# Kernel optimization log

Measured on AMD Instinct MI355X. Metric: run time of the kernel, lower is better.

Reference implementation:

```python
import jax, jax.numpy as jnp
import numpy as np

B, N, C, H = 4, 2048, 1024, 16
D = C // H  # head_dim


def setup_inputs() -> dict:
    key = jax.random.key(0)
    ks = jax.random.split(key, 9)
    s = 1.0 / np.sqrt(C)
    return {
        "x": jax.random.normal(ks[0], (B, N, C), dtype=jnp.float32),
        "Wq": jax.random.uniform(ks[1], (C, C), jnp.float32, -s, s),
        "bq": jax.random.uniform(ks[2], (C,), jnp.float32, -s, s),
        "Wk": jax.random.uniform(ks[3], (C, C), jnp.float32, -s, s),
        "bk": jax.random.uniform(ks[4], (C,), jnp.float32, -s, s),
        "Wv": jax.random.uniform(ks[5], (C, C), jnp.float32, -s, s),
        "bv": jax.random.uniform(ks[6], (C,), jnp.float32, -s, s),
        "Wo": jax.random.uniform(ks[7], (C, C), jnp.float32, -s, s),
        "bo": jax.random.uniform(ks[8], (C,), jnp.float32, -s, s),
    }


def reference(x, Wq, bq, Wk, bk, Wv, bv, Wo, bo):
    # QKV projections -> [B, H, N, D]
    def proj(W, b):
        y = jnp.einsum('bnc,cd->bnd', x, W) + b
        return y.reshape(B, N, H, D).transpose(0, 2, 1, 3)

    q = proj(Wq, bq)
    k = proj(Wk, bk)
    v = proj(Wv, bv)

    scale = 1.0 / np.sqrt(D).astype(np.float32)
    scores = jnp.einsum('bhnd,bhmd->bhnm', q, k) * scale  # [B,H,N,N]
    probs = jax.nn.softmax(scores, axis=-1)
    out = jnp.einsum('bhnm,bhmd->bhnd', probs, v)  # [B,H,N,D]
    out = out.transpose(0, 2, 1, 3).reshape(B, N, C)
    return jnp.einsum('bnc,cd->bnd', out, Wo) + bo
```

## Files before the change

### kernel.cpp

```cpp
#include <hip/hip_runtime.h>
#include <hip/hip_bf16.h>
#include <stdint.h>


#define DEV __device__ __forceinline__

typedef unsigned short u16;
typedef __attribute__((ext_vector_type(8))) _Float16 f16x8;
typedef __attribute__((ext_vector_type(4))) float f32x4;

static constexpr int NB = 4, NN = 2048, NC = 1024, NH = 16, ND = 64;

DEV u16 f2h(float f) {
    _Float16 h = (_Float16)f;
    return __builtin_bit_cast(u16, h);
}

#define GLD16(gp, lp)                                                         \
    __builtin_amdgcn_global_load_lds(                                         \
        (__attribute__((address_space(1))) void*)(gp),                        \
        (__attribute__((address_space(3))) void*)(lp), 16, 0, 0)

DEV f32x4 mfma16(f16x8 a, f16x8 b, f32x4 c) {
    return __builtin_amdgcn_mfma_f32_16x16x32_f16(a, b, c, 0, 0, 0);
}

__global__ void cast_fuse(const float* __restrict__ x,
                          const float* __restrict__ Wq, const float* __restrict__ Wk,
                          const float* __restrict__ Wv, const float* __restrict__ Wo,
                          u16* __restrict__ xb, u16* __restrict__ Wt4) {
    __shared__ float lds[64 * 68];
    int bid = blockIdx.x, tid = threadIdx.x;
    if (bid < 4096) {
        size_t base = (size_t)bid * 2048 + (size_t)tid * 8;
        float4 v0 = *(const float4*)(x + base);
        float4 v1 = *(const float4*)(x + base + 4);
        union { u16 u[8]; uint4 v; } p;
        p.u[0] = f2h(v0.x); p.u[1] = f2h(v0.y); p.u[2] = f2h(v0.z); p.u[3] = f2h(v0.w);
        p.u[4] = f2h(v1.x); p.u[5] = f2h(v1.y); p.u[6] = f2h(v1.z); p.u[7] = f2h(v1.w);
        *(uint4*)(xb + base) = p.v;
        return;
    }
    bid -= 4096;
    int wsel = bid >> 8, t = bid & 255;
    int k0 = (t >> 4) * 64, n0 = (t & 15) * 64;
    const float* W = wsel == 0 ? Wq : wsel == 1 ? Wk : wsel == 2 ? Wv : Wo;
    u16* Wt = Wt4 + (size_t)wsel * 1048576;
#pragma unroll
    for (int i = 0; i < 4; i++) {
        int slot = tid * 4 + i * 1024;
        int rr = slot >> 6, cc = slot & 63;
        float4 v = *(const float4*)(W + (size_t)(k0 + rr) * 1024 + n0 + cc);
        *(float4*)(&lds[rr * 68 + cc]) = v;
    }
    __syncthreads();
    int n = tid >> 2, kc = (tid & 3) * 16;
    union { u16 u[16]; uint4 v[2]; } p;
#pragma unroll
    for (int j = 0; j < 16; j++) p.u[j] = f2h(lds[(kc + j) * 68 + n]);
    u16* dst = Wt + (size_t)(n0 + n) * 1024 + k0 + kc;
    *(uint4*)(dst) = p.v[0];
    *(uint4*)(dst + 8) = p.v[1];
}

DEV void gemm_core(const u16* __restrict__ A, const u16* __restrict__ Wt,
                   int m0, int n0, f32x4 (&acc)[4][4]) {
    __shared__ u16 Alds[128 * 32];
    __shared__ u16 Blds[128 * 32];
    const int tid = threadIdx.x, lane = tid & 63;
    const int w = tid >> 6, g = lane >> 4, r16 = lane & 15;
    const int wm = (w >> 1) * 64, wn = (w & 1) * 64;
#pragma unroll
    for (int i = 0; i < 4; i++)
#pragma unroll
        for (int j = 0; j < 4; j++) acc[i][j] = f32x4{0.f, 0.f, 0.f, 0.f};

    for (int kt = 0; kt < 32; ++kt) {
        int k0 = kt * 32;
#pragma unroll
        for (int i = 0; i < 2; i++) {
            int slot = i * 4096 + tid * 16;
            int rr = slot >> 6, cc = slot & 63;
            GLD16((const char*)A + (size_t)(m0 + rr) * 2048 + k0 * 2 + cc,
                  (char*)Alds + slot);
            GLD16((const char*)Wt + (size_t)(n0 + rr) * 2048 + k0 * 2 + cc,
                  (char*)Blds + slot);
        }
        __syncthreads();
        f16x8 af[4], bf[4];
#pragma unroll
        for (int i = 0; i < 4; i++) {
            af[i] = *(const f16x8*)((const char*)Alds + (wm + i * 16 + r16) * 64 + g * 16);
            bf[i] = *(const f16x8*)((const char*)Blds + (wn + i * 16 + r16) * 64 + g * 16);
        }
#pragma unroll
        for (int i = 0; i < 4; i++)
#pragma unroll
            for (int j = 0; j < 4; j++) acc[i][j] = mfma16(af[i], bf[j], acc[i][j]);
        __syncthreads();
    }
}

__global__ __launch_bounds__(256, 2) void gemm_qkv(
    const u16* __restrict__ xb, const u16* __restrict__ Wt4,
    const float* __restrict__ bq, const float* __restrict__ bk,
    const float* __restrict__ bv,
    u16* __restrict__ Qo, u16* __restrict__ Ko, u16* __restrict__ Vo) {
    int m0 = blockIdx.x * 128, n0 = blockIdx.y * 128, z = blockIdx.z;
    const u16* Wt = Wt4 + (size_t)z * 1048576;
    const float* bias = z == 0 ? bq : z == 1 ? bk : bv;
    u16* Out = z == 0 ? Qo : z == 1 ? Ko : Vo;
    f32x4 acc[4][4];
    gemm_core(xb, Wt, m0, n0, acc);
    const int lane = threadIdx.x & 63, w = threadIdx.x >> 6;
    const int g = lane >> 4, r16 = lane & 15;
    const int wm = (w >> 1) * 64, wn = (w & 1) * 64;
#pragma unroll
    for (int j = 0; j < 4; j++) {
        int c = n0 + wn + j * 16 + r16;
        float bb = bias[c];
        int h = c >> 6, d = c & 63;
#pragma unroll
        for (int i = 0; i < 4; i++) {
#pragma unroll
            for (int rr = 0; rr < 4; rr++) {
                int m = m0 + wm + i * 16 + g * 4 + rr;
                int b = m >> 11, n = m & 2047;
                Out[(((size_t)(b * 16 + h)) * 2048 + n) * 64 + d] = f2h(acc[i][j][rr] + bb);
            }
        }
    }
}

__global__ __launch_bounds__(256, 2) void gemm_out(
    const u16* __restrict__ AO, const u16* __restrict__ Wt,
    const float* __restrict__ bo, float* __restrict__ Out) {
    int m0 = blockIdx.x * 128, n0 = blockIdx.y * 128;
    f32x4 acc[4][4];
    gemm_core(AO, Wt, m0, n0, acc);
    const int lane = threadIdx.x & 63, w = threadIdx.x >> 6;
    const int g = lane >> 4, r16 = lane & 15;
    const int wm = (w >> 1) * 64, wn = (w & 1) * 64;
#pragma unroll
    for (int j = 0; j < 4; j++) {
        int c = n0 + wn + j * 16 + r16;
        float bb = bo[c];
#pragma unroll
        for (int i = 0; i < 4; i++) {
#pragma unroll
            for (int rr = 0; rr < 4; rr++) {
                int m = m0 + wm + i * 16 + g * 4 + rr;
                Out[(size_t)m * 1024 + c] = acc[i][j][rr] + bb;
            }
        }
    }
}

__global__ void transpose_v(const u16* __restrict__ V, u16* __restrict__ VT) {
    __shared__ u16 lds[64 * 66];
    int bh = blockIdx.x >> 5, n0 = (blockIdx.x & 31) * 64;
    const u16* Vb = V + (size_t)bh * 2048 * 64;
    u16* VTb = VT + (size_t)bh * 64 * 2048;
    int tid = threadIdx.x;
#pragma unroll
    for (int i = 0; i < 8; i++) {
        int p = tid + i * 256;
        int rr = p >> 5, c2 = (p & 31) * 2;
        unsigned int val = *(const unsigned int*)(Vb + (size_t)(n0 + rr) * 64 + c2);
        *(unsigned int*)(&lds[rr * 66 + c2]) = val;
    }
    __syncthreads();
#pragma unroll
    for (int i = 0; i < 2; i++) {
        int s = tid * 8 + i * 2048;
        int d = s >> 6, ns = s & 63;
        union { u16 u[8]; uint4 v; } p;
#pragma unroll
        for (int j = 0; j < 8; j++) p.u[j] = lds[(ns + j) * 66 + d];
        *(uint4*)(VTb + (size_t)d * 2048 + n0 + ns) = p.v;
    }
}

__global__ __launch_bounds__(256, 2) void attn_k(
    const u16* __restrict__ Q, const u16* __restrict__ K,
    const u16* __restrict__ VT, u16* __restrict__ AO) {
    __shared__ char Klds[8192];
    __shared__ char Vlds[8192];
    __shared__ char Plds[4][4096];
    const int bh = blockIdx.x, q0 = blockIdx.y * 128;
    const int tid = threadIdx.x, lane = tid & 63, w = tid >> 6;
    const int g = lane >> 4, r16 = lane & 15;
    const char* Qb = (const char*)(Q + (size_t)bh * 2048 * 64);
    const char* Kb = (const char*)(K + (size_t)bh * 2048 * 64);
    const char* VTb = (const char*)(VT + (size_t)bh * 64 * 2048);

    f16x8 qf[2][2];
#pragma unroll
    for (int qg = 0; qg < 2; qg++)
#pragma unroll
        for (int ks = 0; ks < 2; ks++)
            qf[qg][ks] = *(const f16x8*)(Qb + (size_t)(q0 + w * 32 + qg * 16 + r16) * 128 +
                                         ks * 64 + g * 16);
    f32x4 oacc[2][4];
#pragma unroll
    for (int qg = 0; qg < 2; qg++)
#pragma unroll
        for (int dg = 0; dg < 4; dg++) oacc[qg][dg] = f32x4{0.f, 0.f, 0.f, 0.f};
    float mrun[2] = {-1e30f, -1e30f}, lrun[2] = {0.f, 0.f};

    for (int t = 0; t < 32; ++t) {
#pragma unroll
        for (int i = 0; i < 2; i++) {
            int slot = i * 4096 + tid * 16;
            int rr = slot >> 7, cc = slot & 127;
            int sw = cc ^ ((rr & 7) << 4);
            GLD16(Kb + (size_t)(t * 64 + rr) * 128 + sw, Klds + slot);
            GLD16(VTb + (size_t)rr * 4096 + t * 128 + sw, Vlds + slot);
        }
        __syncthreads();

        f32x4 sacc[4][2];
#pragma unroll
        for (int kg = 0; kg < 4; kg++)
#pragma unroll
            for (int qg = 0; qg < 2; qg++) sacc[kg][qg] = f32x4{0.f, 0.f, 0.f, 0.f};
#pragma unroll
        for (int kg = 0; kg < 4; kg++) {
#pragma unroll
            for (int ks = 0; ks < 2; ks++) {
                int row = kg * 16 + r16;
                f16x8 kf = *(const f16x8*)(Klds + row * 128 +
                                           ((ks * 64 + g * 16) ^ ((row & 7) << 4)));
#pragma unroll
                for (int qg = 0; qg < 2; qg++)
                    sacc[kg][qg] = mfma16(kf, qf[qg][ks], sacc[kg][qg]);
            }
        }

#pragma unroll
        for (int qg = 0; qg < 2; qg++) {
            float pm = -1e30f;
#pragma unroll
            for (int kg = 0; kg < 4; kg++)
#pragma unroll
                for (int rr = 0; rr < 4; rr++) pm = fmaxf(pm, sacc[kg][qg][rr]);
            pm = fmaxf(pm, __shfl_xor(pm, 16));
            pm = fmaxf(pm, __shfl_xor(pm, 32));
            pm *= 0.125f;
            float mn = fmaxf(mrun[qg], pm);
            float fsc = exp2f((mrun[qg] - mn) * 1.44269504f);
            mrun[qg] = mn;
            float nm = -mn * 1.44269504f;
            float rs = 0.f;
#pragma unroll
            for (int kg = 0; kg < 4; kg++) {
                union { u16 u[4]; uint2 v; } pk;
#pragma unroll
                for (int rr = 0; rr < 4; rr++) {
                    float p = exp2f(fmaf(sacc[kg][qg][rr], 0.18033688f, nm));
                    rs += p;
                    pk.u[rr] = f2h(p);
                }
                int byte = (qg * 16 + r16) * 128 + ((kg * 32 + g * 8) ^ ((r16 & 7) << 4));
                *(uint2*)(&Plds[w][byte]) = pk.v;
            }
            rs += __shfl_xor(rs, 16);
            rs += __shfl_xor(rs, 32);
            lrun[qg] = lrun[qg] * fsc + rs;
            float fr[4];
#pragma unroll
            for (int rr = 0; rr < 4; rr++) fr[rr] = __shfl(fsc, g * 4 + rr);
#pragma unroll
            for (int dg = 0; dg < 4; dg++)
#pragma unroll
                for (int rr = 0; rr < 4; rr++) oacc[qg][dg][rr] *= fr[rr];
        }

#pragma unroll
        for (int ks = 0; ks < 2; ks++) {
            f16x8 pf[2], vf[4];
#pragma unroll
            for (int qg = 0; qg < 2; qg++) {
                int row = qg * 16 + r16;
                pf[qg] = *(const f16x8*)(Plds[w] + row * 128 +
                                         ((ks * 64 + g * 16) ^ ((r16 & 7) << 4)));
            }
#pragma unroll
            for (int dg = 0; dg < 4; dg++) {
                int row = dg * 16 + r16;
                vf[dg] = *(const f16x8*)(Vlds + row * 128 +
                                         ((ks * 64 + g * 16) ^ ((r16 & 7) << 4)));
            }
#pragma unroll
            for (int qg = 0; qg < 2; qg++)
#pragma unroll
                for (int dg = 0; dg < 4; dg++)
                    oacc[qg][dg] = mfma16(pf[qg], vf[dg], oacc[qg][dg]);
        }
        __syncthreads();
    }

    const int b = bh >> 4, h = bh & 15;
#pragma unroll
    for (int qg = 0; qg < 2; qg++) {
        float linv = 1.0f / lrun[qg];
        float lr[4];
#pragma unroll
        for (int rr = 0; rr < 4; rr++) lr[rr] = __shfl(linv, g * 4 + rr);
#pragma unroll
        for (int dg = 0; dg < 4; dg++) {
            int d = dg * 16 + r16;
#pragma unroll
            for (int rr = 0; rr < 4; rr++) {
                int nrow = q0 + w * 32 + qg * 16 + g * 4 + rr;
                AO[((size_t)(b * 2048 + nrow)) * 1024 + h * 64 + d] =
                    f2h(oacc[qg][dg][rr] * lr[rr]);
            }
        }
    }
}

extern "C" void kernel_launch(void* const* d_in, const int* in_sizes, int n_in,
                              void* d_out, int out_size, void* d_ws, size_t ws_size,
                              hipStream_t stream) {
    const float* x = (const float*)d_in[0];
    const float* Wq = (const float*)d_in[1];
    const float* bq = (const float*)d_in[2];
    const float* Wk = (const float*)d_in[3];
    const float* bk = (const float*)d_in[4];
    const float* Wv = (const float*)d_in[5];
    const float* bv = (const float*)d_in[6];
    const float* Wo = (const float*)d_in[7];
    const float* bo = (const float*)d_in[8];

    char* ws = (char*)d_ws;
    u16* xb  = (u16*)(ws);
    u16* Wt  = (u16*)(ws + (16ull << 20));
    u16* Qb  = (u16*)(ws + (24ull << 20));
    u16* Kb  = (u16*)(ws + (40ull << 20));
    u16* Vb  = (u16*)(ws + (56ull << 20));
    u16* VTb = (u16*)(ws + (72ull << 20));
    u16* AO  = (u16*)(ws + (88ull << 20));

    cast_fuse<<<dim3(5120), dim3(256), 0, stream>>>(x, Wq, Wk, Wv, Wo, xb, Wt);
    gemm_qkv<<<dim3(64, 8, 3), dim3(256), 0, stream>>>(xb, Wt, bq, bk, bv, Qb, Kb, Vb);
    transpose_v<<<dim3(2048), dim3(256), 0, stream>>>(Vb, VTb);
    attn_k<<<dim3(64, 16), dim3(256), 0, stream>>>(Qb, Kb, VTb, AO);
    gemm_out<<<dim3(64, 8), dim3(256), 0, stream>>>(AO, Wt + 3ull * 1048576, bo,
                                                    (float*)d_out);
}
```

Baseline: 345.1 us.

## Double-buffer GEMM and attention tiles, widen KV tile, lazy softmax rescale

Both the projection GEMM core and the attention kernel now stage the next tile into a second LDS buffer while computing on the current one, so there is only one barrier per iteration. The attention kernel processes 128 keys per step and raises wave priority around the MFMA sections. It rescales the running max and output only when some row's max grows by more than a threshold. The 1/sqrt(D) scale is folded into the Q projection epilogue. The cost is more LDS per block (about 80 KB for attention), which may limit occupancy, and extra register pressure from the larger score tile.

```diff
diff --git a/kernel.cpp b/kernel.cpp
--- a/kernel.cpp
+++ b/kernel.cpp
@@ -8,8 +8,6 @@
 typedef unsigned short u16;
 typedef __attribute__((ext_vector_type(8))) _Float16 f16x8;
 typedef __attribute__((ext_vector_type(4))) float f32x4;
-
-static constexpr int NB = 4, NN = 2048, NC = 1024, NH = 16, ND = 64;
 
 DEV u16 f2h(float f) {
     _Float16 h = (_Float16)f;
@@ -65,8 +63,8 @@
 
 DEV void gemm_core(const u16* __restrict__ A, const u16* __restrict__ Wt,
                    int m0, int n0, f32x4 (&acc)[4][4]) {
-    __shared__ u16 Alds[128 * 32];
-    __shared__ u16 Blds[128 * 32];
+    __shared__ u16 Alds[2][128 * 32];
+    __shared__ u16 Blds[2][128 * 32];
     const int tid = threadIdx.x, lane = tid & 63;
     const int w = tid >> 6, g = lane >> 4, r16 = lane & 15;
     const int wm = (w >> 1) * 64, wn = (w & 1) * 64;
@@ -75,23 +73,29 @@
 #pragma unroll
         for (int j = 0; j < 4; j++) acc[i][j] = f32x4{0.f, 0.f, 0.f, 0.f};
 
-    for (int kt = 0; kt < 32; ++kt) {
-        int k0 = kt * 32;
+    auto stage = [&](int buf, int kt) {
+        int k0 = kt * 64;
 #pragma unroll
         for (int i = 0; i < 2; i++) {
             int slot = i * 4096 + tid * 16;
             int rr = slot >> 6, cc = slot & 63;
-            GLD16((const char*)A + (size_t)(m0 + rr) * 2048 + k0 * 2 + cc,
-                  (char*)Alds + slot);
-            GLD16((const char*)Wt + (size_t)(n0 + rr) * 2048 + k0 * 2 + cc,
-                  (char*)Blds + slot);
-        }
-        __syncthreads();
+            GLD16((const char*)A + (size_t)(m0 + rr) * 2048 + k0 + cc,
+                  (char*)Alds[buf] + slot);
+            GLD16((const char*)Wt + (size_t)(n0 + rr) * 2048 + k0 + cc,
+                  (char*)Blds[buf] + slot);
+        }
+    };
+    stage(0, 0);
+    __syncthreads();
+
+    for (int kt = 0; kt < 32; ++kt) {
+        int cur = kt & 1;
+        if (kt < 31) stage(cur ^ 1, kt + 1);
         f16x8 af[4], bf[4];
 #pragma unroll
         for (int i = 0; i < 4; i++) {
-            af[i] = *(const f16x8*)((const char*)Alds + (wm + i * 16 + r16) * 64 + g * 16);
-            bf[i] = *(const f16x8*)((const char*)Blds + (wn + i * 16 + r16) * 64 + g * 16);
+            af[i] = *(const f16x8*)((const char*)Alds[cur] + (wm + i * 16 + r16) * 64 + g * 16);
+            bf[i] = *(const f16x8*)((const char*)Blds[cur] + (wn + i * 16 + r16) * 64 + g * 16);
         }
 #pragma unroll
         for (int i = 0; i < 4; i++)
@@ -110,6 +114,7 @@
     const u16* Wt = Wt4 + (size_t)z * 1048576;
     const float* bias = z == 0 ? bq : z == 1 ? bk : bv;
     u16* Out = z == 0 ? Qo : z == 1 ? Ko : Vo;
+    const float sc = (z == 0) ? 0.125f : 1.0f;
     f32x4 acc[4][4];
     gemm_core(xb, Wt, m0, n0, acc);
     const int lane = threadIdx.x & 63, w = threadIdx.x >> 6;
@@ -126,7 +131,8 @@
             for (int rr = 0; rr < 4; rr++) {
                 int m = m0 + wm + i * 16 + g * 4 + rr;
                 int b = m >> 11, n = m & 2047;
-                Out[(((size_t)(b * 16 + h)) * 2048 + n) * 64 + d] = f2h(acc[i][j][rr] + bb);
+                Out[(((size_t)(b * 16 + h)) * 2048 + n) * 64 + d] =
+                    f2h((acc[i][j][rr] + bb) * sc);
             }
         }
     }
@@ -184,8 +190,8 @@
 __global__ __launch_bounds__(256, 2) void attn_k(
     const u16* __restrict__ Q, const u16* __restrict__ K,
     const u16* __restrict__ VT, u16* __restrict__ AO) {
-    __shared__ char Klds[8192];
-    __shared__ char Vlds[8192];
+    __shared__ char Klds[2][16384];
+    __shared__ char Vlds[2][16384];
     __shared__ char Plds[4][4096];
     const int bh = blockIdx.x, q0 = blockIdx.y * 128;
     const int tid = threadIdx.x, lane = tid & 63, w = tid >> 6;
@@ -193,6 +199,8 @@
     const char* Qb = (const char*)(Q + (size_t)bh * 2048 * 64);
     const char* Kb = (const char*)(K + (size_t)bh * 2048 * 64);
     const char* VTb = (const char*)(VT + (size_t)bh * 64 * 2048);
+    char* Pw = Plds[w];
+    const f32x4 ZZ = {0.f, 0.f, 0.f, 0.f};
 
     f16x8 qf[2][2];
 #pragma unroll
@@ -205,98 +213,128 @@
 #pragma unroll
     for (int qg = 0; qg < 2; qg++)
 #pragma unroll
-        for (int dg = 0; dg < 4; dg++) oacc[qg][dg] = f32x4{0.f, 0.f, 0.f, 0.f};
+        for (int dg = 0; dg < 4; dg++) oacc[qg][dg] = ZZ;
     float mrun[2] = {-1e30f, -1e30f}, lrun[2] = {0.f, 0.f};
 
-    for (int t = 0; t < 32; ++t) {
-#pragma unroll
-        for (int i = 0; i < 2; i++) {
+    auto stage = [&](int buf, int t) {
+#pragma unroll
+        for (int i = 0; i < 4; i++) {
             int slot = i * 4096 + tid * 16;
-            int rr = slot >> 7, cc = slot & 127;
-            int sw = cc ^ ((rr & 7) << 4);
-            GLD16(Kb + (size_t)(t * 64 + rr) * 128 + sw, Klds + slot);
-            GLD16(VTb + (size_t)rr * 4096 + t * 128 + sw, Vlds + slot);
-        }
-        __syncthreads();
-
-        f32x4 sacc[4][2];
-#pragma unroll
-        for (int kg = 0; kg < 4; kg++)
-#pragma unroll
-            for (int qg = 0; qg < 2; qg++) sacc[kg][qg] = f32x4{0.f, 0.f, 0.f, 0.f};
-#pragma unroll
-        for (int kg = 0; kg < 4; kg++) {
-#pragma unroll
-            for (int ks = 0; ks < 2; ks++) {
-                int row = kg * 16 + r16;
-                f16x8 kf = *(const f16x8*)(Klds + row * 128 +
-                                           ((ks * 64 + g * 16) ^ ((row & 7) << 4)));
-#pragma unroll
-                for (int qg = 0; qg < 2; qg++)
-                    sacc[kg][qg] = mfma16(kf, qf[qg][ks], sacc[kg][qg]);
-            }
-        }
-
+            {
+                int rr = slot >> 7, cc = slot & 127;
+                GLD16(Kb + (size_t)(t * 128 + rr) * 128 + (cc ^ ((rr & 7) << 4)),
+                      Klds[buf] + slot);
+            }
+            {
+                int rr = slot >> 8, cc = slot & 255;
+                GLD16(VTb + (size_t)rr * 4096 + t * 256 + (cc ^ ((rr & 7) << 4)),
+                      Vlds[buf] + slot);
+            }
+        }
+    };
+    stage(0, 0);
+    __syncthreads();
+
+    for (int t = 0; t < 16; ++t) {
+        const int cur = t & 1;
+        if (t < 15) stage(cur ^ 1, t + 1);
+        const char* Kl = Klds[cur];
+        const char* Vl = Vlds[cur];
+
+        f32x4 sacc[8][2];
+        __builtin_amdgcn_s_setprio(1);
+#pragma unroll
+        for (int kg = 0; kg < 8; kg++) {
+            int row = kg * 16 + r16, sw = (row & 7) << 4;
+            f16x8 kf0 = *(const f16x8*)(Kl + row * 128 + ((g * 16) ^ sw));
+            f16x8 kf1 = *(const f16x8*)(Kl + row * 128 + ((64 + g * 16) ^ sw));
+#pragma unroll
+            for (int qg = 0; qg < 2; qg++) {
+                sacc[kg][qg] = mfma16(kf0, qf[qg][0], ZZ);
+                sacc[kg][qg] = mfma16(kf1, qf[qg][1], sacc[kg][qg]);
+            }
+        }
+        __builtin_amdgcn_s_setprio(0);
+
+        float pmv[2];
 #pragma unroll
         for (int qg = 0; qg < 2; qg++) {
             float pm = -1e30f;
 #pragma unroll
-            for (int kg = 0; kg < 4; kg++)
+            for (int kg = 0; kg < 8; kg++)
 #pragma unroll
                 for (int rr = 0; rr < 4; rr++) pm = fmaxf(pm, sacc[kg][qg][rr]);
             pm = fmaxf(pm, __shfl_xor(pm, 16));
             pm = fmaxf(pm, __shfl_xor(pm, 32));
-            pm *= 0.125f;
-            float mn = fmaxf(mrun[qg], pm);
-            float fsc = exp2f((mrun[qg] - mn) * 1.44269504f);
-            mrun[qg] = mn;
-            float nm = -mn * 1.44269504f;
-            float rs = 0.f;
-#pragma unroll
-            for (int kg = 0; kg < 4; kg++) {
-                union { u16 u[4]; uint2 v; } pk;
-#pragma unroll
-                for (int rr = 0; rr < 4; rr++) {
-                    float p = exp2f(fmaf(sacc[kg][qg][rr], 0.18033688f, nm));
-                    rs += p;
-                    pk.u[rr] = f2h(p);
+            pmv[qg] = pm;
+        }
+        if (__any(fmaxf(pmv[0] - mrun[0], pmv[1] - mrun[1]) > 8.0f)) {
+#pragma unroll
+            for (int qg = 0; qg < 2; qg++) {
+                float mn = fmaxf(mrun[qg], pmv[qg]);
+                float fsc = exp2f((mrun[qg] - mn) * 1.44269504f);
+                mrun[qg] = mn;
+                lrun[qg] *= fsc;
+                float fr[4];
+#pragma unroll
+                for (int rr = 0; rr < 4; rr++) fr[rr] = __shfl(fsc, g * 4 + rr);
+#pragma unroll
+                for (int dg = 0; dg < 4; dg++)
+#pragma unroll
+                    for (int rr = 0; rr < 4; rr++) oacc[qg][dg][rr] *= fr[rr];
+            }
+        }
+
+        float rs[2] = {0.f, 0.f};
+#pragma unroll
+        for (int h = 0; h < 2; h++) {
+#pragma unroll
+            for (int qg = 0; qg < 2; qg++) {
+                float nm = -mrun[qg] * 1.44269504f;
+#pragma unroll
+                for (int kg2 = 0; kg2 < 4; kg2++) {
+                    int kg = h * 4 + kg2;
+                    union { u16 u[4]; uint2 v; } pk;
+#pragma unroll
+                    for (int rr = 0; rr < 4; rr++) {
+                        float p = exp2f(fmaf(sacc[kg][qg][rr], 1.44269504f, nm));
+                        rs[qg] += p;
+                        pk.u[rr] = f2h(p);
+                    }
+                    *(uint2*)(Pw + (qg * 16 + r16) * 128 +
+                              ((kg2 * 32 + g * 8) ^ ((r16 & 7) << 4))) = pk.v;
                 }
-                int byte = (qg * 16 + r16) * 128 + ((kg * 32 + g * 8) ^ ((r16 & 7) << 4));
-                *(uint2*)(&Plds[w][byte]) = pk.v;
-            }
-            rs += __shfl_xor(rs, 16);
-            rs += __shfl_xor(rs, 32);
-            lrun[qg] = lrun[qg] * fsc + rs;
-            float fr[4];
-#pragma unroll
-            for (int rr = 0; rr < 4; rr++) fr[rr] = __shfl(fsc, g * 4 + rr);
-#pragma unroll
-            for (int dg = 0; dg < 4; dg++)
-#pragma unroll
-                for (int rr = 0; rr < 4; rr++) oacc[qg][dg][rr] *= fr[rr];
-        }
-
-#pragma unroll
-        for (int ks = 0; ks < 2; ks++) {
-            f16x8 pf[2], vf[4];
-#pragma unroll
-            for (int qg = 0; qg < 2; qg++) {
-                int row = qg * 16 + r16;
-                pf[qg] = *(const f16x8*)(Plds[w] + row * 128 +
-                                         ((ks * 64 + g * 16) ^ ((r16 & 7) << 4)));
-            }
-#pragma unroll
-            for (int dg = 0; dg < 4; dg++) {
-                int row = dg * 16 + r16;
-                vf[dg] = *(const f16x8*)(Vlds + row * 128 +
-                                         ((ks * 64 + g * 16) ^ ((r16 & 7) << 4)));
-            }
-#pragma unroll
-            for (int qg = 0; qg < 2; qg++)
-#pragma unroll
-                for (int dg = 0; dg < 4; dg++)
-                    oacc[qg][dg] = mfma16(pf[qg], vf[dg], oacc[qg][dg]);
-        }
+            }
+            __builtin_amdgcn_s_setprio(1);
+#pragma unroll
+            for (int ks2 = 0; ks2 < 2; ks2++) {
+                f16x8 pf[2], vf[4];
+#pragma unroll
+                for (int qg = 0; qg < 2; qg++) {
+                    int row = qg * 16 + r16;
+                    pf[qg] = *(const f16x8*)(Pw + row * 128 +
+                                             ((ks2 * 64 + g * 16) ^ ((r16 & 7) << 4)));
+                }
+#pragma unroll
+                for (int dg = 0; dg < 4; dg++) {
+                    int row = dg * 16 + r16;
+                    vf[dg] = *(const f16x8*)(Vl + row * 256 +
+                                             ((h * 128 + ks2 * 64 + g * 16) ^ ((row & 7) << 4)));
+                }
+#pragma unroll
+                for (int qg = 0; qg < 2; qg++)
+#pragma unroll
+                    for (int dg = 0; dg < 4; dg++)
+                        oacc[qg][dg] = mfma16(pf[qg], vf[dg], oacc[qg][dg]);
+            }
+            __builtin_amdgcn_s_setprio(0);
+        }
+        rs[0] += __shfl_xor(rs[0], 16);
+        rs[0] += __shfl_xor(rs[0], 32);
+        rs[1] += __shfl_xor(rs[1], 16);
+        rs[1] += __shfl_xor(rs[1], 32);
+        lrun[0] += rs[0];
+        lrun[1] += rs[1];
         __syncthreads();
     }
 
```

Measured after the change: 332.7 us. -3.6%, faster.
